# Kernel optimization log

Hardware: AMD Instinct MI355X
Metric: run time of the kernel (lower is better)

The kernel has to match this reference:

```python
import jax, jax.numpy as jnp
import numpy as np

N, OUT, IN = 16384, 2048, 2048

def setup_inputs() -> dict:
    key = jax.random.key(0)
    k1, k2, k3 = jax.random.split(key, 3)
    input_ = jax.random.normal(k1, (N, IN), dtype=jnp.float32)
    # kaiming normal, fan_in mode: std = sqrt(2/fan_in)
    weight = jax.random.normal(k2, (OUT, IN), dtype=jnp.float32) * np.sqrt(2.0 / IN)
    mask = jax.random.randint(k3, (OUT, IN), 0, 2, dtype=jnp.int32)
    return {"input_": input_, "weight": weight, "mask": mask}

def reference(input_, weight, mask):
    # out = x @ (W * mask)^T  -- mask is a fixed binary expander pattern
    masked_w = weight * mask.astype(weight.dtype)  # [OUT, IN]
    return jnp.matmul(input_, masked_w.T)          # [N, OUT]
```

## Files before the change

kernel.cpp:

```cpp
#include <hip/hip_runtime.h>


#define MDIM 16384
#define NDIM 2048
#define KDIM 2048

#define BM 256
#define BN 128
#define GRID_X ((MDIM / BM) * (NDIM / BN))

using f32x4   = __attribute__((ext_vector_type(4))) float;
using bf16x8  = __attribute__((ext_vector_type(8))) __bf16;
using ushort8 = __attribute__((ext_vector_type(8))) unsigned short;

__device__ __forceinline__ unsigned short f2bf(float f) {
  unsigned int u = __builtin_bit_cast(unsigned int, f);
  u = u + 0x7FFFu + ((u >> 16) & 1u);
  return (unsigned short)(u >> 16);
}


__global__ void convert_input_kernel(const float* __restrict__ in,
                                     unsigned short* __restrict__ out) {
  size_t base = ((size_t)blockIdx.x * blockDim.x + threadIdx.x) * 8;
  float4 a = *reinterpret_cast<const float4*>(in + base);
  float4 b = *reinterpret_cast<const float4*>(in + base + 4);
  ushort8 v;
  v[0] = f2bf(a.x); v[1] = f2bf(a.y); v[2] = f2bf(a.z); v[3] = f2bf(a.w);
  v[4] = f2bf(b.x); v[5] = f2bf(b.y); v[6] = f2bf(b.z); v[7] = f2bf(b.w);
  *reinterpret_cast<ushort8*>(out + base) = v;
}

__global__ void convert_weight_kernel(const float* __restrict__ w,
                                      const int* __restrict__ mk,
                                      unsigned short* __restrict__ out) {
  size_t base = ((size_t)blockIdx.x * blockDim.x + threadIdx.x) * 8;
  float4 a = *reinterpret_cast<const float4*>(w + base);
  float4 b = *reinterpret_cast<const float4*>(w + base + 4);
  int4 m0 = *reinterpret_cast<const int4*>(mk + base);
  int4 m1 = *reinterpret_cast<const int4*>(mk + base + 4);
  ushort8 v;
  v[0] = m0.x ? f2bf(a.x) : (unsigned short)0;
  v[1] = m0.y ? f2bf(a.y) : (unsigned short)0;
  v[2] = m0.z ? f2bf(a.z) : (unsigned short)0;
  v[3] = m0.w ? f2bf(a.w) : (unsigned short)0;
  v[4] = m1.x ? f2bf(b.x) : (unsigned short)0;
  v[5] = m1.y ? f2bf(b.y) : (unsigned short)0;
  v[6] = m1.z ? f2bf(b.z) : (unsigned short)0;
  v[7] = m1.w ? f2bf(b.w) : (unsigned short)0;
  *reinterpret_cast<ushort8*>(out + base) = v;
}


__device__ __forceinline__ f32x4 MF(bf16x8 a, bf16x8 b, f32x4 c) {
  return __builtin_amdgcn_mfma_f32_16x16x32_bf16(a, b, c, 0, 0, 0);
}
__device__ __forceinline__ void bar() {
  asm volatile("" ::: "memory");
  __builtin_amdgcn_s_barrier();
  asm volatile("" ::: "memory");
}
#define VMCNT(n) asm volatile("s_waitcnt vmcnt(" #n ")" ::: "memory")

__global__ __launch_bounds__(512, 4) void gemm_tlp(
    const unsigned short* __restrict__ Abf,
    const unsigned short* __restrict__ Bbf,
    float* __restrict__ C) {
  __shared__ __attribute__((aligned(16))) unsigned short Asl[3 * 8192];
  __shared__ __attribute__((aligned(16))) unsigned short Bsl[2 * 4096];

  int bid = blockIdx.x;
  int wgs = (bid & 7) * (GRID_X / 8) + (bid >> 3);
  int tm = wgs >> 4;
  int tn = wgs & 15;
  int row0 = tm * BM, col0 = tn * BN;

  int t = threadIdx.x;
  int lane = t & 63, wid = t >> 6;
  int wr = wid >> 1, wc = wid & 1;
  int fr = lane & 15, fq = lane >> 4;

  int p0 = (wid * 2) * 64 + lane;
  int ra0 = p0 >> 2, ka0 = ((p0 & 3) ^ ((ra0 >> 1) & 3)) * 8;
  int p1 = p0 + 64;
  int ra1 = p1 >> 2, ka1 = ((p1 & 3) ^ ((ra1 >> 1) & 3)) * 8;
  size_t offA0 = (size_t)(row0 + ra0) * KDIM + ka0;
  size_t offA1 = (size_t)(row0 + ra1) * KDIM + ka1;
  int ldswA0 = (wid * 2) * 512, ldswA1 = (wid * 2 + 1) * 512;
  int q = wid * 64 + lane;
  int rb = q >> 2, kb_ = ((q & 3) ^ ((rb >> 1) & 3)) * 8;
  size_t offB0 = (size_t)(col0 + rb) * KDIM + kb_;
  int ldswB = wid * 512;

  int kxor = (fq ^ ((fr >> 1) & 3)) * 8;
  int aoff = (wr * 64 + fr) * 32 + kxor;
  int boff = (wc * 64 + fr) * 32 + kxor;

  f32x4 acc[4][4];
#pragma unroll
  for (int m = 0; m < 4; ++m)
#pragma unroll
    for (int n = 0; n < 4; ++n) acc[m][n] = f32x4{0.f, 0.f, 0.f, 0.f};

#define STGA(sa, ke) do {                                                       \
  __builtin_amdgcn_global_load_lds(                                             \
      (const __attribute__((address_space(1))) void*)(Abf + offA0 + (ke)),      \
      (__attribute__((address_space(3))) void*)(Asl + (sa) * 8192 + ldswA0),    \
      16, 0, 0);                                                                \
  __builtin_amdgcn_global_load_lds(                                             \
      (const __attribute__((address_space(1))) void*)(Abf + offA1 + (ke)),      \
      (__attribute__((address_space(3))) void*)(Asl + (sa) * 8192 + ldswA1),    \
      16, 0, 0);                                                                \
} while (0)
#define STGB(sb, ke) do {                                                       \
  __builtin_amdgcn_global_load_lds(                                             \
      (const __attribute__((address_space(1))) void*)(Bbf + offB0 + (ke)),      \
      (__attribute__((address_space(3))) void*)(Bsl + (sb) * 4096 + ldswB),     \
      16, 0, 0);                                                                \
} while (0)

#define PH(sa, sb, STAGES, WAITS) do {                                          \
  STAGES;                                                                       \
  WAITS;                                                                        \
  bar();                                                                        \
  const unsigned short* _ap = Asl + (sa) * 8192 + aoff;                         \
  const unsigned short* _bp = Bsl + (sb) * 4096 + boff;                         \
  bf16x8 _af[4], _bf[4];                                                        \
  _Pragma("unroll")                                                             \
  for (int _m = 0; _m < 4; ++_m) _af[_m] = *(const bf16x8*)(_ap + _m * 512);    \
  _Pragma("unroll")                                                             \
  for (int _n = 0; _n < 4; ++_n) _bf[_n] = *(const bf16x8*)(_bp + _n * 512);    \
  __builtin_amdgcn_s_setprio(1);                                                \
  _Pragma("unroll")                                                             \
  for (int _m = 0; _m < 4; ++_m)                                                \
    _Pragma("unroll")                                                           \
    for (int _n = 0; _n < 4; ++_n)                                              \
      acc[_m][_n] = MF(_af[_m], _bf[_n], acc[_m][_n]);                          \
  __builtin_amdgcn_s_setprio(0);                                                \
  bar();                                                                        \
} while (0)

  STGA(0, 0);
  STGA(1, 32);
  STGB(0, 0);

  for (int i = 0; i < 10; ++i) {
    int kb = i * 192;
    PH(0, 0, { STGA(2, kb + 64);  STGB(1, kb + 32);  }, VMCNT(3));
    PH(1, 1, { STGA(0, kb + 96);  STGB(0, kb + 64);  }, VMCNT(3));
    PH(2, 0, { STGA(1, kb + 128); STGB(1, kb + 96);  }, VMCNT(3));
    PH(0, 1, { STGA(2, kb + 160); STGB(0, kb + 128); }, VMCNT(3));
    PH(1, 0, { STGA(0, kb + 192); STGB(1, kb + 160); }, VMCNT(3));
    PH(2, 1, { STGA(1, kb + 224); STGB(0, kb + 192); }, VMCNT(3));
  }
  PH(0, 0, { STGA(2, 1984); STGB(1, 1952); }, VMCNT(3));
  PH(1, 1, { STGA(0, 2016); STGB(0, 1984); }, VMCNT(3));
  PH(2, 0, { STGB(1, 2016); }, VMCNT(1));
  PH(0, 1, , VMCNT(0));

  size_t crow = (size_t)(row0 + wr * 64 + fq * 4);
  int ccol = col0 + wc * 64 + fr;
#pragma unroll
  for (int m = 0; m < 4; ++m)
#pragma unroll
    for (int n = 0; n < 4; ++n) {
      float* cp = C + (crow + m * 16) * NDIM + ccol + n * 16;
#pragma unroll
      for (int e = 0; e < 4; ++e) cp[(size_t)e * NDIM] = acc[m][n][e];
    }
#undef PH
#undef STGA
#undef STGB
}


__global__ __launch_bounds__(256) void gemm_fused_fallback(
    const float* __restrict__ Afp,
    const float* __restrict__ Wfp,
    const int* __restrict__ Mk,
    float* __restrict__ C) {
  __shared__ unsigned short As[128 * 32];
  __shared__ unsigned short Bs[128 * 32];
  int bid = blockIdx.x;
  int nwg = (MDIM / 128) * (NDIM / 128);
  int wg = (bid & 7) * (nwg / 8) + (bid >> 3);
  int tm = wg >> 4, tn = wg & 15;
  int row0 = tm * 128, col0 = tn * 128;
  int t = threadIdx.x;
  int lane = t & 63, wv = t >> 6;
  int wr = wv >> 1, wc = wv & 1;
  int fr = lane & 15, fq = lane >> 4;
  f32x4 acc[4][4];
#pragma unroll
  for (int i = 0; i < 4; ++i)
#pragma unroll
    for (int j = 0; j < 4; ++j) acc[i][j] = f32x4{0.f, 0.f, 0.f, 0.f};
  for (int kt = 0; kt < KDIM; kt += 32) {
#pragma unroll
    for (int j = 0; j < 2; ++j) {
      int c = j * 256 + t;
      int r = c >> 2;
      int ko = (c & 3) * 8;
      const float* ga = Afp + (size_t)(row0 + r) * KDIM + kt + ko;
      float4 a0 = *reinterpret_cast<const float4*>(ga);
      float4 a1 = *reinterpret_cast<const float4*>(ga + 4);
      ushort8 va;
      va[0] = f2bf(a0.x); va[1] = f2bf(a0.y); va[2] = f2bf(a0.z); va[3] = f2bf(a0.w);
      va[4] = f2bf(a1.x); va[5] = f2bf(a1.y); va[6] = f2bf(a1.z); va[7] = f2bf(a1.w);
      *reinterpret_cast<ushort8*>(As + (size_t)c * 8) = va;
      const float* gw = Wfp + (size_t)(col0 + r) * KDIM + kt + ko;
      const int* gm = Mk + (size_t)(col0 + r) * KDIM + kt + ko;
      float4 w0 = *reinterpret_cast<const float4*>(gw);
      float4 w1 = *reinterpret_cast<const float4*>(gw + 4);
      int4 m0 = *reinterpret_cast<const int4*>(gm);
      int4 m1 = *reinterpret_cast<const int4*>(gm + 4);
      ushort8 vb;
      vb[0] = m0.x ? f2bf(w0.x) : (unsigned short)0;
      vb[1] = m0.y ? f2bf(w0.y) : (unsigned short)0;
      vb[2] = m0.z ? f2bf(w0.z) : (unsigned short)0;
      vb[3] = m0.w ? f2bf(w0.w) : (unsigned short)0;
      vb[4] = m1.x ? f2bf(w1.x) : (unsigned short)0;
      vb[5] = m1.y ? f2bf(w1.y) : (unsigned short)0;
      vb[6] = m1.z ? f2bf(w1.z) : (unsigned short)0;
      vb[7] = m1.w ? f2bf(w1.w) : (unsigned short)0;
      *reinterpret_cast<ushort8*>(Bs + (size_t)c * 8) = vb;
    }
    __syncthreads();
    bf16x8 af[4], bfr[4];
#pragma unroll
    for (int m2 = 0; m2 < 4; ++m2)
      af[m2] = *reinterpret_cast<const bf16x8*>(As + (wr * 64 + m2 * 16 + fr) * 32 + fq * 8);
#pragma unroll
    for (int n2 = 0; n2 < 4; ++n2)
      bfr[n2] = *reinterpret_cast<const bf16x8*>(Bs + (wc * 64 + n2 * 16 + fr) * 32 + fq * 8);
#pragma unroll
    for (int m2 = 0; m2 < 4; ++m2)
#pragma unroll
      for (int n2 = 0; n2 < 4; ++n2)
        acc[m2][n2] = MF(af[m2], bfr[n2], acc[m2][n2]);
    __syncthreads();
  }
#pragma unroll
  for (int m2 = 0; m2 < 4; ++m2)
#pragma unroll
    for (int n2 = 0; n2 < 4; ++n2) {
      size_t r0 = (size_t)(row0 + wr * 64 + m2 * 16 + fq * 4);
      size_t c0 = (size_t)(col0 + wc * 64 + n2 * 16 + fr);
#pragma unroll
      for (int i = 0; i < 4; ++i) C[(r0 + i) * NDIM + c0] = acc[m2][n2][i];
    }
}


extern "C" void kernel_launch(void* const* d_in, const int* in_sizes, int n_in,
                              void* d_out, int out_size, void* d_ws, size_t ws_size,
                              hipStream_t stream) {
  const float* input  = (const float*)d_in[0];
  const float* weight = (const float*)d_in[1];
  const int*   mask   = (const int*)d_in[2];
  float* out = (float*)d_out;

  const size_t needA = (size_t)MDIM * KDIM * sizeof(unsigned short);
  const size_t needB = (size_t)NDIM * KDIM * sizeof(unsigned short);

  if (ws_size >= needA + needB) {
    unsigned short* Abf = (unsigned short*)d_ws;
    unsigned short* Bbf = (unsigned short*)((char*)d_ws + needA);
    convert_input_kernel<<<(MDIM * (size_t)KDIM / 8) / 256, 256, 0, stream>>>(input, Abf);
    convert_weight_kernel<<<(NDIM * (size_t)KDIM / 8) / 256, 256, 0, stream>>>(weight, mask, Bbf);
    gemm_tlp<<<GRID_X, 512, 0, stream>>>(Abf, Bbf, out);
  } else {
    int nwg = (MDIM / 128) * (NDIM / 128);
    gemm_fused_fallback<<<nwg, 256, 0, stream>>>(input, weight, mask, out);
  }
}
```

Baseline: 187.3 us.

## Enlarge GEMM tile to 256x256 and load B fragments straight into registers

The GEMM tile grows from 256x128 to 256x256, with each wave computing a 128x64 block (8x4 MFMA accumulators). B is no longer staged through LDS: each wave loads its B fragments from global memory into double-buffered registers. A uses a 4-stage LDS ring instead of 3 stages. This raises arithmetic intensity and removes B's LDS traffic and barriers. In exchange it needs far more registers, which drops occupancy to 2 blocks per CU, and the uncoalesced direct global B loads may add latency.

```diff
diff --git a/kernel.cpp b/kernel.cpp
--- a/kernel.cpp
+++ b/kernel.cpp
@@ -6,7 +6,7 @@
 #define KDIM 2048
 
 #define BM 256
-#define BN 128
+#define BN 256
 #define GRID_X ((MDIM / BM) * (NDIM / BN))
 
 using f32x4   = __attribute__((ext_vector_type(4))) float;
@@ -62,106 +62,103 @@
 }
 #define VMCNT(n) asm volatile("s_waitcnt vmcnt(" #n ")" ::: "memory")
 
-__global__ __launch_bounds__(512, 4) void gemm_tlp(
+__global__ __launch_bounds__(512, 2) void gemm_breg(
     const unsigned short* __restrict__ Abf,
     const unsigned short* __restrict__ Bbf,
     float* __restrict__ C) {
-  __shared__ __attribute__((aligned(16))) unsigned short Asl[3 * 8192];
-  __shared__ __attribute__((aligned(16))) unsigned short Bsl[2 * 4096];
+  __shared__ __attribute__((aligned(16))) unsigned short Asl[4 * 8192];
 
   int bid = blockIdx.x;
   int wgs = (bid & 7) * (GRID_X / 8) + (bid >> 3);
-  int tm = wgs >> 4;
-  int tn = wgs & 15;
+  int tm = wgs >> 3;
+  int tn = wgs & 7;
   int row0 = tm * BM, col0 = tn * BN;
 
   int t = threadIdx.x;
   int lane = t & 63, wid = t >> 6;
-  int wr = wid >> 1, wc = wid & 1;
+  int wr = wid >> 2, wc = wid & 3;
   int fr = lane & 15, fq = lane >> 4;
 
   int p0 = (wid * 2) * 64 + lane;
-  int ra0 = p0 >> 2, ka0 = ((p0 & 3) ^ ((ra0 >> 1) & 3)) * 8;
-  int p1 = p0 + 64;
-  int ra1 = p1 >> 2, ka1 = ((p1 & 3) ^ ((ra1 >> 1) & 3)) * 8;
-  size_t offA0 = (size_t)(row0 + ra0) * KDIM + ka0;
-  size_t offA1 = (size_t)(row0 + ra1) * KDIM + ka1;
-  int ldswA0 = (wid * 2) * 512, ldswA1 = (wid * 2 + 1) * 512;
-  int q = wid * 64 + lane;
-  int rb = q >> 2, kb_ = ((q & 3) ^ ((rb >> 1) & 3)) * 8;
-  size_t offB0 = (size_t)(col0 + rb) * KDIM + kb_;
-  int ldswB = wid * 512;
+  int r0 = p0 >> 2, kc0 = ((p0 & 3) ^ ((r0 >> 1) & 3)) * 8;
+  size_t offA0 = (size_t)(row0 + r0) * KDIM + kc0;
+  int ldsw0 = (wid * 2) * 512;
 
   int kxor = (fq ^ ((fr >> 1) & 3)) * 8;
-  int aoff = (wr * 64 + fr) * 32 + kxor;
-  int boff = (wc * 64 + fr) * 32 + kxor;
-
-  f32x4 acc[4][4];
-#pragma unroll
-  for (int m = 0; m < 4; ++m)
+  int aoff = (wr * 128 + fr) * 32 + kxor;
+
+  size_t offB = (size_t)(col0 + wc * 64 + fr) * KDIM + fq * 8;
+  const unsigned short* bp0 = Bbf + offB;
+  const unsigned short* bp1 = bp0 + 16 * KDIM;
+  const unsigned short* bp2 = bp0 + 32 * KDIM;
+  const unsigned short* bp3 = bp0 + 48 * KDIM;
+
+  f32x4 acc[8][4];
+#pragma unroll
+  for (int m = 0; m < 8; ++m)
 #pragma unroll
     for (int n = 0; n < 4; ++n) acc[m][n] = f32x4{0.f, 0.f, 0.f, 0.f};
+
+  bf16x8 afr[8], bP[4], bQ[4];
 
 #define STGA(sa, ke) do {                                                       \
   __builtin_amdgcn_global_load_lds(                                             \
       (const __attribute__((address_space(1))) void*)(Abf + offA0 + (ke)),      \
-      (__attribute__((address_space(3))) void*)(Asl + (sa) * 8192 + ldswA0),    \
+      (__attribute__((address_space(3))) void*)(Asl + (sa) * 8192 + ldsw0),     \
       16, 0, 0);                                                                \
   __builtin_amdgcn_global_load_lds(                                             \
-      (const __attribute__((address_space(1))) void*)(Abf + offA1 + (ke)),      \
-      (__attribute__((address_space(3))) void*)(Asl + (sa) * 8192 + ldswA1),    \
+      (const __attribute__((address_space(1))) void*)(Abf + offA0 + 32768 +     \
+                                                      (ke)),                    \
+      (__attribute__((address_space(3))) void*)(Asl + (sa) * 8192 + ldsw0 +     \
+                                                512),                           \
       16, 0, 0);                                                                \
 } while (0)
-#define STGB(sb, ke) do {                                                       \
-  __builtin_amdgcn_global_load_lds(                                             \
-      (const __attribute__((address_space(1))) void*)(Bbf + offB0 + (ke)),      \
-      (__attribute__((address_space(3))) void*)(Bsl + (sb) * 4096 + ldswB),     \
-      16, 0, 0);                                                                \
+
+#define LDB(BUF, ke) do {                                                       \
+  BUF[0] = *(const bf16x8*)(bp0 + (ke));                                        \
+  BUF[1] = *(const bf16x8*)(bp1 + (ke));                                        \
+  BUF[2] = *(const bf16x8*)(bp2 + (ke));                                        \
+  BUF[3] = *(const bf16x8*)(bp3 + (ke));                                        \
 } while (0)
 
-#define PH(sa, sb, STAGES, WAITS) do {                                          \
+#define PH(sa, BC, BL, STAGES, WAITS) do {                                      \
   STAGES;                                                                       \
   WAITS;                                                                        \
   bar();                                                                        \
   const unsigned short* _ap = Asl + (sa) * 8192 + aoff;                         \
-  const unsigned short* _bp = Bsl + (sb) * 4096 + boff;                         \
-  bf16x8 _af[4], _bf[4];                                                        \
   _Pragma("unroll")                                                             \
-  for (int _m = 0; _m < 4; ++_m) _af[_m] = *(const bf16x8*)(_ap + _m * 512);    \
-  _Pragma("unroll")                                                             \
-  for (int _n = 0; _n < 4; ++_n) _bf[_n] = *(const bf16x8*)(_bp + _n * 512);    \
+  for (int _m = 0; _m < 8; ++_m) afr[_m] = *(const bf16x8*)(_ap + _m * 512);    \
   __builtin_amdgcn_s_setprio(1);                                                \
   _Pragma("unroll")                                                             \
-  for (int _m = 0; _m < 4; ++_m)                                                \
+  for (int _m = 0; _m < 8; ++_m)                                                \
     _Pragma("unroll")                                                           \
     for (int _n = 0; _n < 4; ++_n)                                              \
-      acc[_m][_n] = MF(_af[_m], _bf[_n], acc[_m][_n]);                          \
+      acc[_m][_n] = MF(afr[_m], BC[_n], acc[_m][_n]);                           \
   __builtin_amdgcn_s_setprio(0);                                                \
   bar();                                                                        \
 } while (0)
 
   STGA(0, 0);
   STGA(1, 32);
-  STGB(0, 0);
-
-  for (int i = 0; i < 10; ++i) {
-    int kb = i * 192;
-    PH(0, 0, { STGA(2, kb + 64);  STGB(1, kb + 32);  }, VMCNT(3));
-    PH(1, 1, { STGA(0, kb + 96);  STGB(0, kb + 64);  }, VMCNT(3));
-    PH(2, 0, { STGA(1, kb + 128); STGB(1, kb + 96);  }, VMCNT(3));
-    PH(0, 1, { STGA(2, kb + 160); STGB(0, kb + 128); }, VMCNT(3));
-    PH(1, 0, { STGA(0, kb + 192); STGB(1, kb + 160); }, VMCNT(3));
-    PH(2, 1, { STGA(1, kb + 224); STGB(0, kb + 192); }, VMCNT(3));
+  STGA(2, 64);
+  LDB(bP, 0);
+
+  for (int i = 0; i < 15; ++i) {
+    int kb = i * 128;
+    PH(0, bP, bQ, { STGA(3, kb + 96);  LDB(bQ, kb + 32);  }, VMCNT(6));
+    PH(1, bQ, bP, { STGA(0, kb + 128); LDB(bP, kb + 64);  }, VMCNT(6));
+    PH(2, bP, bQ, { STGA(1, kb + 160); LDB(bQ, kb + 96);  }, VMCNT(6));
+    PH(3, bQ, bP, { STGA(2, kb + 192); LDB(bP, kb + 128); }, VMCNT(6));
   }
-  PH(0, 0, { STGA(2, 1984); STGB(1, 1952); }, VMCNT(3));
-  PH(1, 1, { STGA(0, 2016); STGB(0, 1984); }, VMCNT(3));
-  PH(2, 0, { STGB(1, 2016); }, VMCNT(1));
-  PH(0, 1, , VMCNT(0));
-
-  size_t crow = (size_t)(row0 + wr * 64 + fq * 4);
+  PH(0, bP, bQ, { STGA(3, 2016); LDB(bQ, 1952); }, VMCNT(6));
+  PH(1, bQ, bP, { LDB(bP, 1984); }, VMCNT(4));
+  PH(2, bP, bQ, { LDB(bQ, 2016); }, VMCNT(4));
+  PH(3, bQ, bP, , VMCNT(0));
+
+  size_t crow = (size_t)(row0 + wr * 128 + fq * 4);
   int ccol = col0 + wc * 64 + fr;
 #pragma unroll
-  for (int m = 0; m < 4; ++m)
+  for (int m = 0; m < 8; ++m)
 #pragma unroll
     for (int n = 0; n < 4; ++n) {
       float* cp = C + (crow + m * 16) * NDIM + ccol + n * 16;
@@ -169,8 +166,8 @@
       for (int e = 0; e < 4; ++e) cp[(size_t)e * NDIM] = acc[m][n][e];
     }
 #undef PH
+#undef LDB
 #undef STGA
-#undef STGB
 }
 
 
@@ -268,7 +265,7 @@
     unsigned short* Bbf = (unsigned short*)((char*)d_ws + needA);
     convert_input_kernel<<<(MDIM * (size_t)KDIM / 8) / 256, 256, 0, stream>>>(input, Abf);
     convert_weight_kernel<<<(NDIM * (size_t)KDIM / 8) / 256, 256, 0, stream>>>(weight, mask, Bbf);
-    gemm_tlp<<<GRID_X, 512, 0, stream>>>(Abf, Bbf, out);
+    gemm_breg<<<GRID_X, 512, 0, stream>>>(Abf, Bbf, out);
   } else {
     int nwg = (MDIM / 128) * (NDIM / 128);
     gemm_fused_fallback<<<nwg, 256, 0, stream>>>(input, weight, mask, out);
```

Result: slower. 234.9 us (+25.4%).
